# Performance work log

Hardware: AMD Instinct MI355X
Metric: run time of the kernel (lower is better)

Reference implementation:

```python
import jax, jax.numpy as jnp
import numpy as np

H_STEP = 0.1  # diffusion step size h


def vector_layer(V, W):
    """V: [B, Cin, 9, N]; W: [Cout, Cin, 6].
    Faithful to torch vectorLayer: per component-group, conv1d with kernel
    covering the 3 group entries == contraction over (Cin, group), then the
    scalar result is broadcast back to the 3 group positions.
    Groups [0,3,6]->W[:,:,:3], [1,4,7]->W[:,:,3:6], [2,5,8]->W[:,:,3:6]."""
    o0 = jnp.einsum('bcgn,ocg->bon', V[:, :, (0, 3, 6), :], W[:, :, 0:3])
    o1 = jnp.einsum('bcgn,ocg->bon', V[:, :, (1, 4, 7), :], W[:, :, 3:6])
    o2 = jnp.einsum('bcgn,ocg->bon', V[:, :, (2, 5, 8), :], W[:, :, 3:6])
    S = jnp.stack([o0, o1, o2], axis=2)          # [B, Cout, 3, N]
    return jnp.tile(S, (1, 1, 3, 1))             # positions i get o_{i%3}


def vector_relu(V, Q):
    """Projection ReLU. V: [B, C, 9, N] viewed as [B, C, 3, 3(xyz), N];
    subtract the ReLU'd projection onto direction Q per 3-vector."""
    B, C, _, N = V.shape
    V5 = V.reshape(B, C, 3, 3, N)
    qnorm = jnp.linalg.norm(Q)
    Qb = (Q / qnorm)[None, None, None, :, None]
    T = jnp.sum(V5 * Q[None, None, None, :, None], axis=3, keepdims=True)
    W = V5 - jax.nn.relu(T / qnorm) * Qb
    return W.reshape(B, C, 9, N)


def double_vector_layer(x, K1, K2, Q):
    x = vector_relu(x, Q)
    x = vector_layer(x, K1)
    x = vector_relu(x, Q)
    x = vector_layer(x, K2)
    return vector_relu(x, Q)


def setup_inputs() -> dict:
    key = jax.random.key(0)
    ks = jax.random.split(key, 12)
    N, E = 8192, 65536
    nNin, nEin, nNopen, nEopen, nNclose, nlayer = 3, 1, 16, 1, 3, 5
    nopen = nNopen + 2 * nEopen   # 18
    nhid = 2 * nopen              # 36
    s = 0.05  # kernel scale for numerical stability over 5 layers
    return {
        'xnV': jax.random.normal(ks[0], (1, nNin, 9, N), jnp.float32),
        'xeV': jax.random.normal(ks[1], (1, nEin, 9, E), jnp.float32),
        'iInd': jax.random.randint(ks[2], (E,), 0, N),
        'jInd': jax.random.randint(ks[3], (E,), 0, N),
        'K1Nopen': s * jax.random.normal(ks[4], (nNopen, nNin, 6), jnp.float32),
        'K2Nopen': s * jax.random.normal(ks[5], (nNopen, nNopen, 6), jnp.float32),
        'K1Eopen': s * jax.random.normal(ks[6], (nEopen, nEin, 6), jnp.float32),
        'K2Eopen': s * jax.random.normal(ks[7], (nEopen, nEopen, 6), jnp.float32),
        'KE1': s * jax.random.normal(ks[8], (nlayer, nhid, nhid, 6), jnp.float32),
        'KE2': s * jax.random.normal(ks[9], (nlayer, nhid, nhid, 6), jnp.float32),
        'KNclose': s * jax.random.normal(ks[10], (nNclose, nopen, 6), jnp.float32),
        'Q': jax.random.normal(ks[11], (3,), jnp.float32),
    }


def reference(xnV, xeV, iInd, jInd, K1Nopen, K2Nopen, K1Eopen, K2Eopen,
              KE1, KE2, KNclose, Q):
    N = xnV.shape[-1]
    nopen = K2Nopen.shape[0] + 2 * K2Eopen.shape[0]

    def node_grad(x):   # node -> edge gather difference
        return x[..., iInd] - x[..., jInd]

    def node_ave(x):    # node -> edge gather average
        return 0.5 * (x[..., iInd] + x[..., jInd])

    def edge_div(g):    # edge -> node signed scatter-add
        z = jnp.zeros(g.shape[:-1] + (N,), g.dtype)
        return z.at[..., iInd].add(g).at[..., jInd].add(-g)

    def edge_ave(g):    # edge -> node averaged scatter-add
        z = jnp.zeros(g.shape[:-1] + (N,), g.dtype)
        return 0.5 * z.at[..., iInd].add(g).at[..., jInd].add(g)

    xn = double_vector_layer(xnV, K1Nopen, K2Nopen, Q)   # [1,16,9,N]
    xe = double_vector_layer(xeV, K1Eopen, K2Eopen, Q)   # [1,1,9,E]
    xn = jnp.concatenate([xn, edge_div(xe), edge_ave(xe)], axis=1)  # [1,18,9,N]

    Flux = None
    for i in range(KE1.shape[0]):  # fixed nlayer=5 structurally distinct weights
        dxe = jnp.concatenate([node_grad(xn), node_ave(xn)], axis=1)  # [1,36,9,E]
        Flux = double_vector_layer(dxe, KE1[i], KE2[i], Q)            # [1,36,9,E]
        dxn = edge_div(Flux[:, :nopen]) + edge_ave(Flux[:, nopen:])   # [1,18,9,N]
        xn = xn - H_STEP * dxn

    out = vector_layer(xn, KNclose)  # [1,3,9,N]
    return out, Flux
```

## Files before the change

kernel.cpp:

```cpp
#include <hip/hip_runtime.h>

#define N_NODES 8192
#define N_EDGES 65536
#define NS 56
#define FS 112

#define XN3_OFF   0
#define SE_OFF    (N_NODES*NS)
#define MIT_OFF   (SE_OFF + N_EDGES*4)
#define K2N_OFF   (MIT_OFF + 5*5760)
#define KNC_OFF   (K2N_OFF + 2*16*16)
#define K2E_OFF   (KNC_OFF + 2*3*18)
#define FLUX_OFF  750320
#define FLUX_END  (FLUX_OFF + N_EDGES*FS)
#define DEG_OFF   FLUX_END
#define RP_OFF    (DEG_OFF + N_NODES)
#define FP_OFF    (RP_OFF + N_NODES + 1)
#define ADJ_OFF   (FP_OFF + N_NODES)

typedef float f32x2 __attribute__((ext_vector_type(2)));

template<int SLOT>
__device__ __forceinline__ float qb(float x) {
    int r = __builtin_amdgcn_update_dpp(0, __float_as_int(x), SLOT * 0x55, 0xf, 0xf, true);
    return __int_as_float(r);
}
__device__ __forceinline__ float qswap2(float x) {
    int r = __builtin_amdgcn_update_dpp(0, __float_as_int(x), 0x4E, 0xf, 0xf, true);
    return __int_as_float(r);
}

__device__ __forceinline__ void vrelu_p(float& a0, f32x2& a12,
                                        float q0, f32x2 q12, float iq2) {
    float t = fmaf(a0, q0, fmaf(a12.x, q12.x, a12.y * q12.y));
    float r = t > 0.f ? t * iq2 : 0.f;
    a0 = fmaf(-r, q0, a0);
    f32x2 nr = {-r, -r};
    a12 = nr * q12 + a12;
}

__device__ __forceinline__ void vrelu3(float& x0, float& x1, float& x2,
                                       float q0, float q1, float q2, float iq2) {
    float t = x0*q0 + x1*q1 + x2*q2;
    float r = t > 0.f ? t*iq2 : 0.f;
    x0 = fmaf(-r, q0, x0);
    x1 = fmaf(-r, q1, x1);
    x2 = fmaf(-r, q2, x2);
}

__device__ __forceinline__ void ld28(const float4* __restrict__ p, float (&d)[28]) {
#pragma unroll
    for (int t = 0; t < 7; ++t) {
        float4 r = p[t];
        d[4*t] = r.x; d[4*t+1] = r.y; d[4*t+2] = r.z; d[4*t+3] = r.w;
    }
}

template<int QS>
__device__ __forceinline__ void matvec_part(const float* __restrict__ mbase, int q,
        const float (&v0)[9], const f32x2 (&v12)[9],
        float (&a0)[9], f32x2 (&a12)[9]) {
    const float* rb = mbase + QS*720 + q*20;
#pragma unroll
    for (int kc = 0; kc < 9; ++kc) {
        float b0 = qb<QS>(v0[kc]);
        f32x2 b12; b12.x = qb<QS>(v12[kc].x); b12.y = qb<QS>(v12[kc].y);
        const float4* rp = (const float4*)(rb + kc*80);
        float4 R0 = rp[0], R1 = rp[1], R2 = rp[2], R3 = rp[3], R4 = rp[4];
        float m0[9] = {R0.x,R0.y,R0.z,R0.w,R1.x,R1.y,R1.z,R1.w,R2.x};
        float mA[9] = {R2.z,R2.w,R3.x,R3.y,R3.z,R3.w,R4.x,R4.y,R4.z};
#pragma unroll
        for (int k = 0; k < 9; ++k) {
            a0[k] = fmaf(m0[k], b0, a0[k]);
            f32x2 mm = {mA[k], mA[k]};
            a12[k] = mm * b12 + a12[k];
        }
    }
}

__global__ void precompute_kernel(const float* __restrict__ K2N,
                                  const float* __restrict__ K2E,
                                  const float* __restrict__ KE1,
                                  const float* __restrict__ KE2,
                                  const float* __restrict__ KNc,
                                  float* __restrict__ ws) {
    int tid = blockIdx.x * blockDim.x + threadIdx.x;
    int nthr = gridDim.x * blockDim.x;
    for (int m = tid; m < 1440; m += nthr) {
        ws[MIT_OFF + m*20 + 9]  = 0.f;
        ws[MIT_OFF + m*20 + 19] = 0.f;
    }
    for (int m = tid; m < 5*1296; m += nthr) {
        int l = m / 1296, oc = m % 1296;
        int o = oc / 36, c = oc % 36;
        int qq = o / 9, k = o % 9;
        const float* p1 = KE1 + (size_t)(l*1296 + oc)*6;
        const float* p2 = KE2 + (size_t)(l*1296 + oc)*6;
        int base = MIT_OFF + l*5760 + (c*4 + qq)*20;
        ws[base + k]             = p1[0] + p1[1] + p1[2];
        ws[base + 10 + k]        = p1[3] + p1[4] + p1[5];
        ws[base + 2880 + k]      = p2[0] + p2[1] + p2[2];
        ws[base + 2880 + 10 + k] = p2[3] + p2[4] + p2[5];
    }
    for (int m = tid; m < 2*256; m += nthr) {
        int s = m / 256, oc = m % 256;
        const float* p = K2N + oc*6 + 3*s;
        ws[K2N_OFF + m] = p[0] + p[1] + p[2];
    }
    for (int m = tid; m < 2*54; m += nthr) {
        int s = m / 54, oc = m % 54;
        const float* p = KNc + oc*6 + 3*s;
        ws[KNC_OFF + m] = p[0] + p[1] + p[2];
    }
    if (tid < 2) {
        const float* p = K2E + 3*tid;
        ws[K2E_OFF + tid] = p[0] + p[1] + p[2];
    }
}

__global__ void zero_i32_kernel(int* __restrict__ p, int n) {
    int t = blockIdx.x * blockDim.x + threadIdx.x;
    if (t < n) p[t] = 0;
}

__global__ void count_kernel(const int* __restrict__ iInd, const int* __restrict__ jInd,
                             int* __restrict__ deg) {
    int e = blockIdx.x * blockDim.x + threadIdx.x;
    if (e >= N_EDGES) return;
    atomicAdd(&deg[iInd[e]], 1);
    atomicAdd(&deg[jInd[e]], 1);
}

__global__ void scan_kernel(const int* __restrict__ deg, int* __restrict__ rowptr,
                            int* __restrict__ fpos) {
    __shared__ int lds[256];
    int t = threadIdx.x;
    int base = t * 32;
    int s = 0;
#pragma unroll
    for (int k = 0; k < 32; ++k) s += deg[base + k];
    lds[t] = s;
    __syncthreads();
    if (t == 0) {
        int run = 0;
        for (int k = 0; k < 256; ++k) { int v = lds[k]; lds[k] = run; run += v; }
        rowptr[N_NODES] = run;
    }
    __syncthreads();
    int off = lds[t];
#pragma unroll
    for (int k = 0; k < 32; ++k) {
        rowptr[base + k] = off;
        fpos[base + k] = off;
        off += deg[base + k];
    }
}

__global__ void fill_kernel(const int* __restrict__ iInd, const int* __restrict__ jInd,
                            int* __restrict__ fpos, int* __restrict__ adj) {
    int e = blockIdx.x * blockDim.x + threadIdx.x;
    if (e >= N_EDGES) return;
    int p = atomicAdd(&fpos[iInd[e]], 1);
    adj[p] = (e << 1);
    p = atomicAdd(&fpos[jInd[e]], 1);
    adj[p] = (e << 1) | 1;
}

__global__ void node_open_kernel(const float* __restrict__ xnV,
                                 const float* __restrict__ Q,
                                 const float* __restrict__ K1N,
                                 const float* __restrict__ ws,
                                 float* __restrict__ xn3) {
    int n = blockIdx.x * blockDim.x + threadIdx.x;
    if (n >= N_NODES) return;
    float q0 = Q[0], q1 = Q[1], q2 = Q[2];
    float iq2 = 1.f / (q0*q0 + q1*q1 + q2*q2);

    float R[3][9];
#pragma unroll
    for (int c = 0; c < 3; ++c)
#pragma unroll
        for (int p = 0; p < 9; ++p)
            R[c][p] = xnV[(c*9 + p)*N_NODES + n];
#pragma unroll
    for (int c = 0; c < 3; ++c)
#pragma unroll
        for (int v = 0; v < 3; ++v)
            vrelu3(R[c][3*v], R[c][3*v+1], R[c][3*v+2], q0, q1, q2, iq2);

    float s[16][3];
#pragma unroll
    for (int o = 0; o < 16; ++o) {
        float a0 = 0.f, a1 = 0.f, a2 = 0.f;
#pragma unroll
        for (int c = 0; c < 3; ++c)
#pragma unroll
            for (int g = 0; g < 3; ++g) {
                a0 = fmaf(R[c][3*g + 0], K1N[(o*3 + c)*6 + g],     a0);
                a1 = fmaf(R[c][3*g + 1], K1N[(o*3 + c)*6 + 3 + g], a1);
                a2 = fmaf(R[c][3*g + 2], K1N[(o*3 + c)*6 + 3 + g], a2);
            }
        s[o][0] = a0; s[o][1] = a1; s[o][2] = a2;
    }
#pragma unroll
    for (int o = 0; o < 16; ++o)
        vrelu3(s[o][0], s[o][1], s[o][2], q0, q1, q2, iq2);

    float u[16][3];
#pragma unroll
    for (int o = 0; o < 16; ++o) {
        float a0 = 0.f, a1 = 0.f, a2 = 0.f;
#pragma unroll
        for (int c = 0; c < 16; ++c) {
            float m0 = ws[K2N_OFF + o*16 + c];
            float mA = ws[K2N_OFF + 256 + o*16 + c];
            a0 = fmaf(m0, s[c][0], a0);
            a1 = fmaf(mA, s[c][1], a1);
            a2 = fmaf(mA, s[c][2], a2);
        }
        u[o][0] = a0; u[o][1] = a1; u[o][2] = a2;
        vrelu3(u[o][0], u[o][1], u[o][2], q0, q1, q2, iq2);
    }

    float* dst = xn3 + n*NS;
#pragma unroll
    for (int o = 0; o < 16; ++o) {
        int base = (o/9)*28 + (o%9)*3;
#pragma unroll
        for (int g = 0; g < 3; ++g)
            dst[base + g] = u[o][g];
    }
    dst[27] = 0.f;
}

__global__ void edge_open_kernel(const float* __restrict__ xeV,
                                 const float* __restrict__ Q,
                                 const float* __restrict__ K1E,
                                 const float* __restrict__ ws,
                                 float4* __restrict__ se4) {
    int e = blockIdx.x * blockDim.x + threadIdx.x;
    if (e >= N_EDGES) return;
    float q0 = Q[0], q1 = Q[1], q2 = Q[2];
    float iq2 = 1.f / (q0*q0 + q1*q1 + q2*q2);

    float R[9];
#pragma unroll
    for (int p = 0; p < 9; ++p) R[p] = xeV[p*N_EDGES + e];
#pragma unroll
    for (int v = 0; v < 3; ++v)
        vrelu3(R[3*v], R[3*v+1], R[3*v+2], q0, q1, q2, iq2);

    float s0 = 0.f, s1 = 0.f, s2 = 0.f;
#pragma unroll
    for (int g = 0; g < 3; ++g) {
        s0 = fmaf(R[3*g + 0], K1E[g],     s0);
        s1 = fmaf(R[3*g + 1], K1E[3 + g], s1);
        s2 = fmaf(R[3*g + 2], K1E[3 + g], s2);
    }
    vrelu3(s0, s1, s2, q0, q1, q2, iq2);
    s0 *= ws[K2E_OFF + 0];
    s1 *= ws[K2E_OFF + 1];
    s2 *= ws[K2E_OFF + 1];
    vrelu3(s0, s1, s2, q0, q1, q2, iq2);
    se4[e] = make_float4(s0, s1, s2, 0.f);
}

__global__ void open_gather_kernel(const float4* __restrict__ se4,
                                   const int* __restrict__ adj,
                                   const int* __restrict__ rowptr,
                                   float* __restrict__ xn3) {
    int n = blockIdx.x * blockDim.x + threadIdx.x;
    if (n >= N_NODES) return;
    int beg = rowptr[n], end = rowptr[n + 1];
    float d0 = 0.f, d1 = 0.f, d2 = 0.f, a0 = 0.f, a1 = 0.f, a2 = 0.f;
    for (int d = beg; d < end; ++d) {
        int ae = adj[d];
        float sgn = (ae & 1) ? -1.f : 1.f;
        float4 s = se4[ae >> 1];
        d0 = fmaf(sgn, s.x, d0); d1 = fmaf(sgn, s.y, d1); d2 = fmaf(sgn, s.z, d2);
        a0 = fmaf(0.5f, s.x, a0); a1 = fmaf(0.5f, s.y, a1); a2 = fmaf(0.5f, s.z, a2);
    }
    float* dst = xn3 + n*NS;
    dst[49] = d0; dst[50] = d1; dst[51] = d2;
    dst[52] = a0; dst[53] = a1; dst[54] = a2;
    dst[55] = 0.f;
}

template<bool WRITE_FLUX>
__global__ __launch_bounds__(256, 4) void edge_compute_kernel(
        const float* __restrict__ xn3,
        const int* __restrict__ iInd, const int* __restrict__ jInd,
        const float* __restrict__ Q,
        const float* __restrict__ mitg,
        float* __restrict__ flux, float* __restrict__ fluxOut) {
    __shared__ float mit[5760];
    {
        const float4* s4 = (const float4*)mitg;
        float4* d4 = (float4*)mit;
        for (int t = threadIdx.x; t < 1440; t += 256) d4[t] = s4[t];
    }
    __syncthreads();

    int tid = blockIdx.x * 256 + threadIdx.x;
    int e = tid >> 2, q = tid & 3;
    float q0 = Q[0];
    f32x2 q12 = {Q[1], Q[2]};
    float iq2 = 1.f / (q0*q0 + q12.x*q12.x + q12.y*q12.y);
    int i = iInd[e], j = jInd[e];
    const float4* xi = (const float4*)(xn3 + i*NS + 28*(q & 1));
    const float4* xj = (const float4*)(xn3 + j*NS + 28*(q & 1));

    float A[28], B[28];
    ld28(xi, A);
    ld28(xj, B);

    bool isAve = q >= 2;
    float sA = isAve ? 0.5f :  1.f;
    float sB = isAve ? 0.5f : -1.f;
    float v0[9]; f32x2 v12[9];
#pragma unroll
    for (int k = 0; k < 9; ++k) {
        v0[k]    = fmaf(sA, A[3*k],   sB * B[3*k]);
        v12[k].x = fmaf(sA, A[3*k+1], sB * B[3*k+1]);
        v12[k].y = fmaf(sA, A[3*k+2], sB * B[3*k+2]);
        vrelu_p(v0[k], v12[k], q0, q12, iq2);
    }

    float a0[9]; f32x2 a12[9];
#pragma unroll
    for (int k = 0; k < 9; ++k) { a0[k] = 0.f; a12[k] = (f32x2){0.f, 0.f}; }
    matvec_part<0>(mit, q, v0, v12, a0, a12);
    matvec_part<1>(mit, q, v0, v12, a0, a12);
    matvec_part<2>(mit, q, v0, v12, a0, a12);
    matvec_part<3>(mit, q, v0, v12, a0, a12);
#pragma unroll
    for (int k = 0; k < 9; ++k) {
        vrelu_p(a0[k], a12[k], q0, q12, iq2);
        v0[k] = a0[k]; v12[k] = a12[k];
        a0[k] = 0.f; a12[k] = (f32x2){0.f, 0.f};
    }
    matvec_part<0>(mit + 2880, q, v0, v12, a0, a12);
    matvec_part<1>(mit + 2880, q, v0, v12, a0, a12);
    matvec_part<2>(mit + 2880, q, v0, v12, a0, a12);
    matvec_part<3>(mit + 2880, q, v0, v12, a0, a12);
#pragma unroll
    for (int k = 0; k < 9; ++k)
        vrelu_p(a0[k], a12[k], q0, q12, iq2);

    float selO = (q < 2) ? 1.f  : 0.5f;
    float selP = (q < 2) ? 0.5f : -1.f;
    float outv[28];
#pragma unroll
    for (int k = 0; k < 9; ++k) {
        float o0 = qswap2(a0[k]);
        float o1 = qswap2(a12[k].x);
        float o2 = qswap2(a12[k].y);
        outv[3*k]   = fmaf(selO, a0[k],    selP * o0);
        outv[3*k+1] = fmaf(selO, a12[k].x, selP * o1);
        outv[3*k+2] = fmaf(selO, a12[k].y, selP * o2);
    }
    outv[27] = 0.f;
    float4* frow = (float4*)(flux + (size_t)e*FS + q*28);
#pragma unroll
    for (int t = 0; t < 7; ++t)
        frow[t] = make_float4(outv[4*t], outv[4*t+1], outv[4*t+2], outv[4*t+3]);

    if (WRITE_FLUX) {
#pragma unroll
        for (int k = 0; k < 9; ++k) {
#pragma unroll
            for (int p = 0; p < 9; ++p) {
                float wv = (p % 3 == 0) ? a0[k] : (p % 3 == 1) ? a12[k].x : a12[k].y;
                fluxOut[((size_t)((9*q + k)*9 + p))*N_EDGES + e] = wv;
            }
        }
    }
}

__global__ __launch_bounds__(64) void node_gather_kernel(
        const float* __restrict__ flux,
        const int* __restrict__ adj, const int* __restrict__ rowptr,
        float* __restrict__ xn3) {
    int n = blockIdx.x;
    int l = threadIdx.x;
    if (l >= 54) return;
    int idx = l + (l >= 27 ? 1 : 0);
    int beg = rowptr[n], end = rowptr[n + 1];
    float acc = 0.f;
    for (int d = beg; d < end; ++d) {
        int ae = adj[d];
        acc += flux[(size_t)(ae >> 1)*FS + (ae & 1)*56 + idx];
    }
    float* x = xn3 + n*NS + idx;
    *x = fmaf(-0.1f, acc, *x);
}

__global__ void close_kernel(const float* __restrict__ xn3,
                             const float* __restrict__ ws,
                             float* __restrict__ out) {
    int n = blockIdx.x * blockDim.x + threadIdx.x;
    if (n >= N_NODES) return;
    const float* x = xn3 + n*NS;
    float o[3][3];
#pragma unroll
    for (int oo = 0; oo < 3; ++oo) {
        float a0 = 0.f, a1 = 0.f, a2 = 0.f;
#pragma unroll
        for (int c = 0; c < 18; ++c) {
            int xidx = (c/9)*28 + (c%9)*3;
            float m0 = ws[KNC_OFF + oo*18 + c];
            float mA = ws[KNC_OFF + 54 + oo*18 + c];
            a0 = fmaf(m0, x[xidx + 0], a0);
            a1 = fmaf(mA, x[xidx + 1], a1);
            a2 = fmaf(mA, x[xidx + 2], a2);
        }
        o[oo][0] = a0; o[oo][1] = a1; o[oo][2] = a2;
    }
#pragma unroll
    for (int oo = 0; oo < 3; ++oo)
#pragma unroll
        for (int p = 0; p < 9; ++p)
            out[(oo*9 + p)*N_NODES + n] = o[oo][p % 3];
}

extern "C" void kernel_launch(void* const* d_in, const int* in_sizes, int n_in,
                              void* d_out, int out_size, void* d_ws, size_t ws_size,
                              hipStream_t stream) {
    const float* xnV = (const float*)d_in[0];
    const float* xeV = (const float*)d_in[1];
    const int*   iInd = (const int*)d_in[2];
    const int*   jInd = (const int*)d_in[3];
    const float* K1N = (const float*)d_in[4];
    const float* K2N = (const float*)d_in[5];
    const float* K1E = (const float*)d_in[6];
    const float* K2E = (const float*)d_in[7];
    const float* KE1 = (const float*)d_in[8];
    const float* KE2 = (const float*)d_in[9];
    const float* KNc = (const float*)d_in[10];
    const float* Q   = (const float*)d_in[11];

    float* ws   = (float*)d_ws;
    float* xn3  = ws + XN3_OFF;
    float4* se4 = (float4*)(ws + SE_OFF);
    float* flux = ws + FLUX_OFF;
    int* wsi    = (int*)d_ws;
    int* deg    = wsi + DEG_OFF;
    int* rowptr = wsi + RP_OFF;
    int* fpos   = wsi + FP_OFF;
    int* adj    = wsi + ADJ_OFF;

    float* out  = (float*)d_out;
    float* fluxOut = out + 3*9*N_NODES;

    precompute_kernel<<<64, 256, 0, stream>>>(K2N, K2E, KE1, KE2, KNc, ws);
    zero_i32_kernel<<<(N_NODES + 255)/256, 256, 0, stream>>>(deg, N_NODES);
    count_kernel<<<N_EDGES/256, 256, 0, stream>>>(iInd, jInd, deg);
    scan_kernel<<<1, 256, 0, stream>>>(deg, rowptr, fpos);
    fill_kernel<<<N_EDGES/256, 256, 0, stream>>>(iInd, jInd, fpos, adj);

    node_open_kernel<<<N_NODES/256, 256, 0, stream>>>(xnV, Q, K1N, ws, xn3);
    edge_open_kernel<<<N_EDGES/256, 256, 0, stream>>>(xeV, Q, K1E, ws, se4);
    open_gather_kernel<<<N_NODES/256, 256, 0, stream>>>(se4, adj, rowptr, xn3);

    for (int l = 0; l < 5; ++l) {
        const float* mitg = ws + MIT_OFF + l*5760;
        if (l == 4)
            edge_compute_kernel<true><<<N_EDGES*4/256, 256, 0, stream>>>(
                xn3, iInd, jInd, Q, mitg, flux, fluxOut);
        else
            edge_compute_kernel<false><<<N_EDGES*4/256, 256, 0, stream>>>(
                xn3, iInd, jInd, Q, mitg, flux, nullptr);
        node_gather_kernel<<<N_NODES, 64, 0, stream>>>(flux, adj, rowptr, xn3);
    }

    close_kernel<<<N_NODES/256, 256, 0, stream>>>(xn3, ws, out);
}
```

Baseline: 312.2 us.

## Scatter edge flux into CSR-ordered slots so node gathers read contiguously

Edge compute now writes each edge's flux rows directly into the slot given by its CSR position for the i and j endpoints, using posI/posJ arrays precomputed in fill. Node gathers then stream contiguous rows without adjacency indirection. The node and edge open kernels are merged into one launch, the deg zeroing is folded into precompute, and the first-stage matvec accumulators are packed into f32x2 pairs. Edge writes become scattered instead of contiguous, trading write locality for read locality.

```diff
diff --git a/kernel.cpp b/kernel.cpp
--- a/kernel.cpp
+++ b/kernel.cpp
@@ -3,20 +3,19 @@
 #define N_NODES 8192
 #define N_EDGES 65536
 #define NS 56
-#define FS 112
 
 #define XN3_OFF   0
-#define SE_OFF    (N_NODES*NS)
-#define MIT_OFF   (SE_OFF + N_EDGES*4)
+#define MIT_OFF   (N_NODES*NS)
 #define K2N_OFF   (MIT_OFF + 5*5760)
 #define KNC_OFF   (K2N_OFF + 2*16*16)
 #define K2E_OFF   (KNC_OFF + 2*3*18)
-#define FLUX_OFF  750320
-#define FLUX_END  (FLUX_OFF + N_EDGES*FS)
+#define FLUX_OFF  488192
+#define FLUX_END  (FLUX_OFF + 2*N_EDGES*56)
 #define DEG_OFF   FLUX_END
 #define RP_OFF    (DEG_OFF + N_NODES)
 #define FP_OFF    (RP_OFF + N_NODES + 1)
-#define ADJ_OFF   (FP_OFF + N_NODES)
+#define POSI_OFF  (FP_OFF + N_NODES)
+#define POSJ_OFF  (POSI_OFF + N_EDGES)
 
 typedef float f32x2 __attribute__((ext_vector_type(2)));
 
@@ -59,19 +58,22 @@
 template<int QS>
 __device__ __forceinline__ void matvec_part(const float* __restrict__ mbase, int q,
         const float (&v0)[9], const f32x2 (&v12)[9],
-        float (&a0)[9], f32x2 (&a12)[9]) {
+        f32x2 (&a0p)[4], float& a0s, f32x2 (&a12)[9]) {
     const float* rb = mbase + QS*720 + q*20;
 #pragma unroll
     for (int kc = 0; kc < 9; ++kc) {
         float b0 = qb<QS>(v0[kc]);
         f32x2 b12; b12.x = qb<QS>(v12[kc].x); b12.y = qb<QS>(v12[kc].y);
+        f32x2 bb0 = {b0, b0};
         const float4* rp = (const float4*)(rb + kc*80);
         float4 R0 = rp[0], R1 = rp[1], R2 = rp[2], R3 = rp[3], R4 = rp[4];
-        float m0[9] = {R0.x,R0.y,R0.z,R0.w,R1.x,R1.y,R1.z,R1.w,R2.x};
+        f32x2 m0p[4] = {{R0.x,R0.y},{R0.z,R0.w},{R1.x,R1.y},{R1.z,R1.w}};
         float mA[9] = {R2.z,R2.w,R3.x,R3.y,R3.z,R3.w,R4.x,R4.y,R4.z};
 #pragma unroll
+        for (int k = 0; k < 4; ++k) a0p[k] = m0p[k] * bb0 + a0p[k];
+        a0s = fmaf(R2.x, b0, a0s);
+#pragma unroll
         for (int k = 0; k < 9; ++k) {
-            a0[k] = fmaf(m0[k], b0, a0[k]);
             f32x2 mm = {mA[k], mA[k]};
             a12[k] = mm * b12 + a12[k];
         }
@@ -83,9 +85,11 @@
                                   const float* __restrict__ KE1,
                                   const float* __restrict__ KE2,
                                   const float* __restrict__ KNc,
-                                  float* __restrict__ ws) {
+                                  float* __restrict__ ws,
+                                  int* __restrict__ deg) {
     int tid = blockIdx.x * blockDim.x + threadIdx.x;
     int nthr = gridDim.x * blockDim.x;
+    if (tid < N_NODES) deg[tid] = 0;
     for (int m = tid; m < 1440; m += nthr) {
         ws[MIT_OFF + m*20 + 9]  = 0.f;
         ws[MIT_OFF + m*20 + 19] = 0.f;
@@ -118,11 +122,6 @@
     }
 }
 
-__global__ void zero_i32_kernel(int* __restrict__ p, int n) {
-    int t = blockIdx.x * blockDim.x + threadIdx.x;
-    if (t < n) p[t] = 0;
-}
-
 __global__ void count_kernel(const int* __restrict__ iInd, const int* __restrict__ jInd,
                              int* __restrict__ deg) {
     int e = blockIdx.x * blockDim.x + threadIdx.x;
@@ -157,116 +156,114 @@
 }
 
 __global__ void fill_kernel(const int* __restrict__ iInd, const int* __restrict__ jInd,
-                            int* __restrict__ fpos, int* __restrict__ adj) {
+                            int* __restrict__ fpos,
+                            int* __restrict__ posI, int* __restrict__ posJ) {
     int e = blockIdx.x * blockDim.x + threadIdx.x;
     if (e >= N_EDGES) return;
-    int p = atomicAdd(&fpos[iInd[e]], 1);
-    adj[p] = (e << 1);
-    p = atomicAdd(&fpos[jInd[e]], 1);
-    adj[p] = (e << 1) | 1;
-}
-
-__global__ void node_open_kernel(const float* __restrict__ xnV,
-                                 const float* __restrict__ Q,
-                                 const float* __restrict__ K1N,
-                                 const float* __restrict__ ws,
-                                 float* __restrict__ xn3) {
-    int n = blockIdx.x * blockDim.x + threadIdx.x;
-    if (n >= N_NODES) return;
+    posI[e] = atomicAdd(&fpos[iInd[e]], 1);
+    posJ[e] = atomicAdd(&fpos[jInd[e]], 1);
+}
+
+__global__ void open_kernel(const float* __restrict__ xnV,
+                            const float* __restrict__ xeV,
+                            const float* __restrict__ Q,
+                            const float* __restrict__ K1N,
+                            const float* __restrict__ K1E,
+                            const float* __restrict__ ws,
+                            const int* __restrict__ posI, const int* __restrict__ posJ,
+                            float* __restrict__ xn3,
+                            float4* __restrict__ seslot) {
     float q0 = Q[0], q1 = Q[1], q2 = Q[2];
     float iq2 = 1.f / (q0*q0 + q1*q1 + q2*q2);
 
-    float R[3][9];
-#pragma unroll
-    for (int c = 0; c < 3; ++c)
-#pragma unroll
-        for (int p = 0; p < 9; ++p)
-            R[c][p] = xnV[(c*9 + p)*N_NODES + n];
-#pragma unroll
-    for (int c = 0; c < 3; ++c)
+    if (blockIdx.x < 32) {
+        int n = blockIdx.x * 256 + threadIdx.x;
+        float R[3][9];
+#pragma unroll
+        for (int c = 0; c < 3; ++c)
+#pragma unroll
+            for (int p = 0; p < 9; ++p)
+                R[c][p] = xnV[(c*9 + p)*N_NODES + n];
+#pragma unroll
+        for (int c = 0; c < 3; ++c)
+#pragma unroll
+            for (int v = 0; v < 3; ++v)
+                vrelu3(R[c][3*v], R[c][3*v+1], R[c][3*v+2], q0, q1, q2, iq2);
+
+        float s[16][3];
+#pragma unroll
+        for (int o = 0; o < 16; ++o) {
+            float a0 = 0.f, a1 = 0.f, a2 = 0.f;
+#pragma unroll
+            for (int c = 0; c < 3; ++c)
+#pragma unroll
+                for (int g = 0; g < 3; ++g) {
+                    a0 = fmaf(R[c][3*g + 0], K1N[(o*3 + c)*6 + g],     a0);
+                    a1 = fmaf(R[c][3*g + 1], K1N[(o*3 + c)*6 + 3 + g], a1);
+                    a2 = fmaf(R[c][3*g + 2], K1N[(o*3 + c)*6 + 3 + g], a2);
+                }
+            s[o][0] = a0; s[o][1] = a1; s[o][2] = a2;
+        }
+#pragma unroll
+        for (int o = 0; o < 16; ++o)
+            vrelu3(s[o][0], s[o][1], s[o][2], q0, q1, q2, iq2);
+
+        float u[16][3];
+#pragma unroll
+        for (int o = 0; o < 16; ++o) {
+            float a0 = 0.f, a1 = 0.f, a2 = 0.f;
+#pragma unroll
+            for (int c = 0; c < 16; ++c) {
+                float m0 = ws[K2N_OFF + o*16 + c];
+                float mA = ws[K2N_OFF + 256 + o*16 + c];
+                a0 = fmaf(m0, s[c][0], a0);
+                a1 = fmaf(mA, s[c][1], a1);
+                a2 = fmaf(mA, s[c][2], a2);
+            }
+            u[o][0] = a0; u[o][1] = a1; u[o][2] = a2;
+            vrelu3(u[o][0], u[o][1], u[o][2], q0, q1, q2, iq2);
+        }
+
+        float* dst = xn3 + n*NS;
+#pragma unroll
+        for (int o = 0; o < 16; ++o) {
+            int base = (o/9)*28 + (o%9)*3;
+#pragma unroll
+            for (int g = 0; g < 3; ++g)
+                dst[base + g] = u[o][g];
+        }
+        dst[27] = 0.f;
+    } else {
+        int e = (blockIdx.x - 32) * 256 + threadIdx.x;
+        float R[9];
+#pragma unroll
+        for (int p = 0; p < 9; ++p) R[p] = xeV[p*N_EDGES + e];
 #pragma unroll
         for (int v = 0; v < 3; ++v)
-            vrelu3(R[c][3*v], R[c][3*v+1], R[c][3*v+2], q0, q1, q2, iq2);
-
-    float s[16][3];
-#pragma unroll
-    for (int o = 0; o < 16; ++o) {
-        float a0 = 0.f, a1 = 0.f, a2 = 0.f;
-#pragma unroll
-        for (int c = 0; c < 3; ++c)
-#pragma unroll
-            for (int g = 0; g < 3; ++g) {
-                a0 = fmaf(R[c][3*g + 0], K1N[(o*3 + c)*6 + g],     a0);
-                a1 = fmaf(R[c][3*g + 1], K1N[(o*3 + c)*6 + 3 + g], a1);
-                a2 = fmaf(R[c][3*g + 2], K1N[(o*3 + c)*6 + 3 + g], a2);
-            }
-        s[o][0] = a0; s[o][1] = a1; s[o][2] = a2;
-    }
-#pragma unroll
-    for (int o = 0; o < 16; ++o)
-        vrelu3(s[o][0], s[o][1], s[o][2], q0, q1, q2, iq2);
-
-    float u[16][3];
-#pragma unroll
-    for (int o = 0; o < 16; ++o) {
-        float a0 = 0.f, a1 = 0.f, a2 = 0.f;
-#pragma unroll
-        for (int c = 0; c < 16; ++c) {
-            float m0 = ws[K2N_OFF + o*16 + c];
-            float mA = ws[K2N_OFF + 256 + o*16 + c];
-            a0 = fmaf(m0, s[c][0], a0);
-            a1 = fmaf(mA, s[c][1], a1);
-            a2 = fmaf(mA, s[c][2], a2);
-        }
-        u[o][0] = a0; u[o][1] = a1; u[o][2] = a2;
-        vrelu3(u[o][0], u[o][1], u[o][2], q0, q1, q2, iq2);
-    }
-
-    float* dst = xn3 + n*NS;
-#pragma unroll
-    for (int o = 0; o < 16; ++o) {
-        int base = (o/9)*28 + (o%9)*3;
-#pragma unroll
-        for (int g = 0; g < 3; ++g)
-            dst[base + g] = u[o][g];
-    }
-    dst[27] = 0.f;
-}
-
-__global__ void edge_open_kernel(const float* __restrict__ xeV,
-                                 const float* __restrict__ Q,
-                                 const float* __restrict__ K1E,
-                                 const float* __restrict__ ws,
-                                 float4* __restrict__ se4) {
-    int e = blockIdx.x * blockDim.x + threadIdx.x;
-    if (e >= N_EDGES) return;
-    float q0 = Q[0], q1 = Q[1], q2 = Q[2];
-    float iq2 = 1.f / (q0*q0 + q1*q1 + q2*q2);
-
-    float R[9];
-#pragma unroll
-    for (int p = 0; p < 9; ++p) R[p] = xeV[p*N_EDGES + e];
-#pragma unroll
-    for (int v = 0; v < 3; ++v)
-        vrelu3(R[3*v], R[3*v+1], R[3*v+2], q0, q1, q2, iq2);
-
-    float s0 = 0.f, s1 = 0.f, s2 = 0.f;
-#pragma unroll
-    for (int g = 0; g < 3; ++g) {
-        s0 = fmaf(R[3*g + 0], K1E[g],     s0);
-        s1 = fmaf(R[3*g + 1], K1E[3 + g], s1);
-        s2 = fmaf(R[3*g + 2], K1E[3 + g], s2);
-    }
-    vrelu3(s0, s1, s2, q0, q1, q2, iq2);
-    s0 *= ws[K2E_OFF + 0];
-    s1 *= ws[K2E_OFF + 1];
-    s2 *= ws[K2E_OFF + 1];
-    vrelu3(s0, s1, s2, q0, q1, q2, iq2);
-    se4[e] = make_float4(s0, s1, s2, 0.f);
-}
-
-__global__ void open_gather_kernel(const float4* __restrict__ se4,
-                                   const int* __restrict__ adj,
+            vrelu3(R[3*v], R[3*v+1], R[3*v+2], q0, q1, q2, iq2);
+
+        float s0 = 0.f, s1 = 0.f, s2 = 0.f;
+#pragma unroll
+        for (int g = 0; g < 3; ++g) {
+            s0 = fmaf(R[3*g + 0], K1E[g],     s0);
+            s1 = fmaf(R[3*g + 1], K1E[3 + g], s1);
+            s2 = fmaf(R[3*g + 2], K1E[3 + g], s2);
+        }
+        vrelu3(s0, s1, s2, q0, q1, q2, iq2);
+        s0 *= ws[K2E_OFF + 0];
+        s1 *= ws[K2E_OFF + 1];
+        s2 *= ws[K2E_OFF + 1];
+        vrelu3(s0, s1, s2, q0, q1, q2, iq2);
+
+        int pi = posI[e], pj = posJ[e];
+        seslot[2*pi]     = make_float4(s0, s1, s2, 0.f);
+        seslot[2*pi + 1] = make_float4(0.5f*s0, 0.5f*s1, 0.5f*s2, 0.f);
+        seslot[2*pj]     = make_float4(-s0, -s1, -s2, 0.f);
+        seslot[2*pj + 1] = make_float4(0.5f*s0, 0.5f*s1, 0.5f*s2, 0.f);
+    }
+}
+
+__global__ void open_gather_kernel(const float4* __restrict__ seslot,
                                    const int* __restrict__ rowptr,
                                    float* __restrict__ xn3) {
     int n = blockIdx.x * blockDim.x + threadIdx.x;
@@ -274,11 +271,10 @@
     int beg = rowptr[n], end = rowptr[n + 1];
     float d0 = 0.f, d1 = 0.f, d2 = 0.f, a0 = 0.f, a1 = 0.f, a2 = 0.f;
     for (int d = beg; d < end; ++d) {
-        int ae = adj[d];
-        float sgn = (ae & 1) ? -1.f : 1.f;
-        float4 s = se4[ae >> 1];
-        d0 = fmaf(sgn, s.x, d0); d1 = fmaf(sgn, s.y, d1); d2 = fmaf(sgn, s.z, d2);
-        a0 = fmaf(0.5f, s.x, a0); a1 = fmaf(0.5f, s.y, a1); a2 = fmaf(0.5f, s.z, a2);
+        float4 dv = seslot[2*d];
+        float4 av = seslot[2*d + 1];
+        d0 += dv.x; d1 += dv.y; d2 += dv.z;
+        a0 += av.x; a1 += av.y; a2 += av.z;
     }
     float* dst = xn3 + n*NS;
     dst[49] = d0; dst[50] = d1; dst[51] = d2;
@@ -290,6 +286,7 @@
 __global__ __launch_bounds__(256, 4) void edge_compute_kernel(
         const float* __restrict__ xn3,
         const int* __restrict__ iInd, const int* __restrict__ jInd,
+        const int* __restrict__ posI, const int* __restrict__ posJ,
         const float* __restrict__ Q,
         const float* __restrict__ mitg,
         float* __restrict__ flux, float* __restrict__ fluxOut) {
@@ -326,41 +323,56 @@
         vrelu_p(v0[k], v12[k], q0, q12, iq2);
     }
 
-    float a0[9]; f32x2 a12[9];
-#pragma unroll
-    for (int k = 0; k < 9; ++k) { a0[k] = 0.f; a12[k] = (f32x2){0.f, 0.f}; }
-    matvec_part<0>(mit, q, v0, v12, a0, a12);
-    matvec_part<1>(mit, q, v0, v12, a0, a12);
-    matvec_part<2>(mit, q, v0, v12, a0, a12);
-    matvec_part<3>(mit, q, v0, v12, a0, a12);
+    f32x2 a0p[4]; float a0s; f32x2 a12[9];
+#pragma unroll
+    for (int k = 0; k < 4; ++k) a0p[k] = (f32x2){0.f, 0.f};
+    a0s = 0.f;
+#pragma unroll
+    for (int k = 0; k < 9; ++k) a12[k] = (f32x2){0.f, 0.f};
+    matvec_part<0>(mit, q, v0, v12, a0p, a0s, a12);
+    matvec_part<1>(mit, q, v0, v12, a0p, a0s, a12);
+    matvec_part<2>(mit, q, v0, v12, a0p, a0s, a12);
+    matvec_part<3>(mit, q, v0, v12, a0p, a0s, a12);
 #pragma unroll
     for (int k = 0; k < 9; ++k) {
-        vrelu_p(a0[k], a12[k], q0, q12, iq2);
-        v0[k] = a0[k]; v12[k] = a12[k];
-        a0[k] = 0.f; a12[k] = (f32x2){0.f, 0.f};
-    }
-    matvec_part<0>(mit + 2880, q, v0, v12, a0, a12);
-    matvec_part<1>(mit + 2880, q, v0, v12, a0, a12);
-    matvec_part<2>(mit + 2880, q, v0, v12, a0, a12);
-    matvec_part<3>(mit + 2880, q, v0, v12, a0, a12);
-#pragma unroll
-    for (int k = 0; k < 9; ++k)
-        vrelu_p(a0[k], a12[k], q0, q12, iq2);
+        float w0 = (k < 8) ? ((k & 1) ? a0p[k>>1].y : a0p[k>>1].x) : a0s;
+        f32x2 w12 = a12[k];
+        vrelu_p(w0, w12, q0, q12, iq2);
+        v0[k] = w0; v12[k] = w12;
+    }
+#pragma unroll
+    for (int k = 0; k < 4; ++k) a0p[k] = (f32x2){0.f, 0.f};
+    a0s = 0.f;
+#pragma unroll
+    for (int k = 0; k < 9; ++k) a12[k] = (f32x2){0.f, 0.f};
+    matvec_part<0>(mit + 2880, q, v0, v12, a0p, a0s, a12);
+    matvec_part<1>(mit + 2880, q, v0, v12, a0p, a0s, a12);
+    matvec_part<2>(mit + 2880, q, v0, v12, a0p, a0s, a12);
+    matvec_part<3>(mit + 2880, q, v0, v12, a0p, a0s, a12);
+
+    float w0[9]; f32x2 w12[9];
+#pragma unroll
+    for (int k = 0; k < 9; ++k) {
+        w0[k] = (k < 8) ? ((k & 1) ? a0p[k>>1].y : a0p[k>>1].x) : a0s;
+        w12[k] = a12[k];
+        vrelu_p(w0[k], w12[k], q0, q12, iq2);
+    }
 
     float selO = (q < 2) ? 1.f  : 0.5f;
     float selP = (q < 2) ? 0.5f : -1.f;
     float outv[28];
 #pragma unroll
     for (int k = 0; k < 9; ++k) {
-        float o0 = qswap2(a0[k]);
-        float o1 = qswap2(a12[k].x);
-        float o2 = qswap2(a12[k].y);
-        outv[3*k]   = fmaf(selO, a0[k],    selP * o0);
-        outv[3*k+1] = fmaf(selO, a12[k].x, selP * o1);
-        outv[3*k+2] = fmaf(selO, a12[k].y, selP * o2);
+        float o0 = qswap2(w0[k]);
+        float o1 = qswap2(w12[k].x);
+        float o2 = qswap2(w12[k].y);
+        outv[3*k]   = fmaf(selO, w0[k],    selP * o0);
+        outv[3*k+1] = fmaf(selO, w12[k].x, selP * o1);
+        outv[3*k+2] = fmaf(selO, w12[k].y, selP * o2);
     }
     outv[27] = 0.f;
-    float4* frow = (float4*)(flux + (size_t)e*FS + q*28);
+    int slot = (q < 2) ? posI[e] : posJ[e];
+    float4* frow = (float4*)(flux + (size_t)slot*56 + (q & 1)*28);
 #pragma unroll
     for (int t = 0; t < 7; ++t)
         frow[t] = make_float4(outv[4*t], outv[4*t+1], outv[4*t+2], outv[4*t+3]);
@@ -370,7 +382,7 @@
         for (int k = 0; k < 9; ++k) {
 #pragma unroll
             for (int p = 0; p < 9; ++p) {
-                float wv = (p % 3 == 0) ? a0[k] : (p % 3 == 1) ? a12[k].x : a12[k].y;
+                float wv = (p % 3 == 0) ? w0[k] : (p % 3 == 1) ? w12[k].x : w12[k].y;
                 fluxOut[((size_t)((9*q + k)*9 + p))*N_EDGES + e] = wv;
             }
         }
@@ -379,19 +391,23 @@
 
 __global__ __launch_bounds__(64) void node_gather_kernel(
         const float* __restrict__ flux,
-        const int* __restrict__ adj, const int* __restrict__ rowptr,
+        const int* __restrict__ rowptr,
         float* __restrict__ xn3) {
     int n = blockIdx.x;
     int l = threadIdx.x;
-    if (l >= 54) return;
-    int idx = l + (l >= 27 ? 1 : 0);
+    if (l >= 56) return;
     int beg = rowptr[n], end = rowptr[n + 1];
-    float acc = 0.f;
-    for (int d = beg; d < end; ++d) {
-        int ae = adj[d];
-        acc += flux[(size_t)(ae >> 1)*FS + (ae & 1)*56 + idx];
-    }
-    float* x = xn3 + n*NS + idx;
+    const float* p = flux + (size_t)beg * 56 + l;
+    float acc = 0.f, acc2 = 0.f;
+    int d = beg;
+    for (; d + 2 <= end; d += 2) {
+        acc  += p[0];
+        acc2 += p[56];
+        p += 112;
+    }
+    if (d < end) acc += p[0];
+    acc += acc2;
+    float* x = xn3 + n*NS + l;
     *x = fmaf(-0.1f, acc, *x);
 }
 
@@ -441,36 +457,35 @@
 
     float* ws   = (float*)d_ws;
     float* xn3  = ws + XN3_OFF;
-    float4* se4 = (float4*)(ws + SE_OFF);
     float* flux = ws + FLUX_OFF;
     int* wsi    = (int*)d_ws;
     int* deg    = wsi + DEG_OFF;
     int* rowptr = wsi + RP_OFF;
     int* fpos   = wsi + FP_OFF;
-    int* adj    = wsi + ADJ_OFF;
+    int* posI   = wsi + POSI_OFF;
+    int* posJ   = wsi + POSJ_OFF;
 
     float* out  = (float*)d_out;
     float* fluxOut = out + 3*9*N_NODES;
 
-    precompute_kernel<<<64, 256, 0, stream>>>(K2N, K2E, KE1, KE2, KNc, ws);
-    zero_i32_kernel<<<(N_NODES + 255)/256, 256, 0, stream>>>(deg, N_NODES);
+    precompute_kernel<<<64, 256, 0, stream>>>(K2N, K2E, KE1, KE2, KNc, ws, deg);
     count_kernel<<<N_EDGES/256, 256, 0, stream>>>(iInd, jInd, deg);
     scan_kernel<<<1, 256, 0, stream>>>(deg, rowptr, fpos);
-    fill_kernel<<<N_EDGES/256, 256, 0, stream>>>(iInd, jInd, fpos, adj);
-
-    node_open_kernel<<<N_NODES/256, 256, 0, stream>>>(xnV, Q, K1N, ws, xn3);
-    edge_open_kernel<<<N_EDGES/256, 256, 0, stream>>>(xeV, Q, K1E, ws, se4);
-    open_gather_kernel<<<N_NODES/256, 256, 0, stream>>>(se4, adj, rowptr, xn3);
+    fill_kernel<<<N_EDGES/256, 256, 0, stream>>>(iInd, jInd, fpos, posI, posJ);
+
+    open_kernel<<<32 + N_EDGES/256, 256, 0, stream>>>(
+        xnV, xeV, Q, K1N, K1E, ws, posI, posJ, xn3, (float4*)flux);
+    open_gather_kernel<<<N_NODES/256, 256, 0, stream>>>((const float4*)flux, rowptr, xn3);
 
     for (int l = 0; l < 5; ++l) {
         const float* mitg = ws + MIT_OFF + l*5760;
         if (l == 4)
             edge_compute_kernel<true><<<N_EDGES*4/256, 256, 0, stream>>>(
-                xn3, iInd, jInd, Q, mitg, flux, fluxOut);
+                xn3, iInd, jInd, posI, posJ, Q, mitg, flux, fluxOut);
         else
             edge_compute_kernel<false><<<N_EDGES*4/256, 256, 0, stream>>>(
-                xn3, iInd, jInd, Q, mitg, flux, nullptr);
-        node_gather_kernel<<<N_NODES, 64, 0, stream>>>(flux, adj, rowptr, xn3);
+                xn3, iInd, jInd, posI, posJ, Q, mitg, flux, nullptr);
+        node_gather_kernel<<<N_NODES, 64, 0, stream>>>(flux, rowptr, xn3);
     }
 
     close_kernel<<<N_NODES/256, 256, 0, stream>>>(xn3, ws, out);
```

After: 307.3 us. No clear change (-1.6%).
